# Performance work log

Hardware: AMD Instinct MI355X
Metric: run time of the kernel (lower is better)

The kernel has to match this reference:

```python
import jax, jax.numpy as jnp
import numpy as np

B, T, F, H = 64, 2048, 64, 160


def setup_inputs() -> dict:
    key = jax.random.key(0)
    ks = jax.random.split(key, 20)
    s = lambda *shape: 0.05
    inp = {
        "x": jax.random.normal(ks[0], (B, T, F), jnp.float32),
        # dilated conv weight [out=F, in=F, k=3]
        "mix_w": jax.random.normal(ks[1], (F, F, 3), jnp.float32) * 0.1,
        # batchnorm (inference) params
        "bn_g": jnp.ones((F,), jnp.float32),
        "bn_b": jnp.zeros((F,), jnp.float32),
        "bn_m": jax.random.normal(ks[2], (F,), jnp.float32) * 0.1,
        "bn_v": jax.random.uniform(ks[3], (F,), jnp.float32, 0.5, 1.5),
        # GRU1: input F -> hidden H (pytorch gate order r, z, n)
        "w_ih1": jax.random.normal(ks[4], (3 * H, F), jnp.float32) * 0.05,
        "w_hh1": jax.random.normal(ks[5], (3 * H, H), jnp.float32) * 0.05,
        "b_ih1": jax.random.normal(ks[6], (3 * H,), jnp.float32) * 0.05,
        "b_hh1": jax.random.normal(ks[7], (3 * H,), jnp.float32) * 0.05,
        # GRU2: hidden H -> hidden H
        "w_ih2": jax.random.normal(ks[8], (3 * H, H), jnp.float32) * 0.05,
        "w_hh2": jax.random.normal(ks[9], (3 * H, H), jnp.float32) * 0.05,
        "b_ih2": jax.random.normal(ks[10], (3 * H,), jnp.float32) * 0.05,
        "b_hh2": jax.random.normal(ks[11], (3 * H,), jnp.float32) * 0.05,
        # head: Linear(H, H//2) -> GELU -> (dropout=identity in eval) -> Linear(H//2, 2)
        "hw1": jax.random.normal(ks[12], (H // 2, H), jnp.float32) * 0.05,
        "hb1": jnp.zeros((H // 2,), jnp.float32),
        "hw2": jax.random.normal(ks[13], (2, H // 2), jnp.float32) * 0.05,
        "hb2": jnp.zeros((2,), jnp.float32),
    }
    return inp


def _gru(z, w_ih, w_hh, b_ih, b_hh):
    # z: [B, T, in]; returns (all hidden states [B, T, H], final hidden [B, H])
    xg = jnp.einsum('bti,gi->btg', z, w_ih) + b_ih  # [B, T, 3H]
    xg = xg.transpose(1, 0, 2)                       # [T, B, 3H]
    h0 = jnp.zeros((z.shape[0], w_hh.shape[1]), z.dtype)

    def step(h, g):
        hg = h @ w_hh.T + b_hh
        xr, xz, xn = jnp.split(g, 3, axis=-1)
        hr, hz, hn = jnp.split(hg, 3, axis=-1)
        r = jax.nn.sigmoid(xr + hr)
        u = jax.nn.sigmoid(xz + hz)
        n = jnp.tanh(xn + r * hn)
        h_new = (1.0 - u) * n + u * h
        return h_new, h_new

    hT, hs = jax.lax.scan(step, h0, xg)
    return hs.transpose(1, 0, 2), hT


def reference(x, mix_w, bn_g, bn_b, bn_m, bn_v,
              w_ih1, w_hh1, b_ih1, b_hh1,
              w_ih2, w_hh2, b_ih2, b_hh2,
              hw1, hb1, hw2, hb2):
    # dilated conv over time: x [B,T,F] -> [B,F,T]
    xc = x.transpose(0, 2, 1)
    y = jax.lax.conv_general_dilated(
        xc, mix_w, window_strides=(1,), padding=[(2, 2)],
        rhs_dilation=(2,), dimension_numbers=('NCH', 'OIH', 'NCH'))
    # batchnorm (inference) + exact GELU
    scale = bn_g / jnp.sqrt(bn_v + 1e-5)
    y = (y - bn_m[:, None]) * scale[:, None] + bn_b[:, None]
    z = jax.nn.gelu(y, approximate=False).transpose(0, 2, 1)  # [B,T,F]

    h1, _ = _gru(z, w_ih1, w_hh1, b_ih1, b_hh1)    # [B,T,H]
    _, h2T = _gru(h1, w_ih2, w_hh2, b_ih2, b_hh2)  # [B,H] (last timestep)

    q = jax.nn.gelu(h2T @ hw1.T + hb1, approximate=False)
    return q @ hw2.T + hb2  # [B, 2]
```

## Files before the change

kernel.cpp:

```cpp
#include <hip/hip_runtime.h>
#include <cmath>

#define BB 64
#define TT 2048
#define FF 64
#define HH 160
#define G3 480
#define TC 128
#define NC (TT / TC)

#define L2E  1.44269504088896340736f
#define TL2E 2.88539008177792681472f

typedef unsigned int u32;
typedef _Float16 half8 __attribute__((ext_vector_type(8)));
typedef _Float16 half2v __attribute__((ext_vector_type(2)));
typedef float f32x4 __attribute__((ext_vector_type(4)));

__device__ __forceinline__ unsigned short f2h(float v) {
    _Float16 h = (_Float16)v;
    return __builtin_bit_cast(unsigned short, h);
}
__device__ __forceinline__ u32 packh2(float a, float b) {
    return (u32)f2h(a) | ((u32)f2h(b) << 16);
}
__device__ __forceinline__ u32 packhh(_Float16 a, _Float16 b) {
    return (u32)__builtin_bit_cast(unsigned short, a)
         | ((u32)__builtin_bit_cast(unsigned short, b) << 16);
}
__device__ __forceinline__ float h2lo(u32 p) {
    return (float)__builtin_bit_cast(half2v, p)[0];
}
__device__ __forceinline__ float h2hi(u32 p) {
    return (float)__builtin_bit_cast(half2v, p)[1];
}
__device__ __forceinline__ float frcp(float v) { return __builtin_amdgcn_rcpf(v); }
#if __has_builtin(__builtin_amdgcn_exp2f)
__device__ __forceinline__ float fexp2(float v) { return __builtin_amdgcn_exp2f(v); }
#else
__device__ __forceinline__ float fexp2(float v) { return __expf(v * 0.69314718055994530942f); }
#endif
__device__ __forceinline__ float gelu_exact(float v) {
    return 0.5f * v * (1.f + erff(v * 0.70710678118654752f));
}
__device__ __forceinline__ void barrier_lgkm() {
    asm volatile("s_waitcnt lgkmcnt(0)\ns_barrier" ::: "memory");
}
__device__ __forceinline__ half8 load_wrow8(const float* p) {
    const float4* q = (const float4*)p;
    float4 a = q[0], b = q[1];
    half8 r;
    r[0] = (_Float16)a.x; r[1] = (_Float16)a.y; r[2] = (_Float16)a.z; r[3] = (_Float16)a.w;
    r[4] = (_Float16)b.x; r[5] = (_Float16)b.y; r[6] = (_Float16)b.z; r[7] = (_Float16)b.w;
    return r;
}
__device__ __forceinline__ half8 load_wrow8s(const float* p, float s) {
    const float4* q = (const float4*)p;
    float4 a = q[0], b = q[1];
    half8 r;
    r[0] = (_Float16)(a.x * s); r[1] = (_Float16)(a.y * s);
    r[2] = (_Float16)(a.z * s); r[3] = (_Float16)(a.w * s);
    r[4] = (_Float16)(b.x * s); r[5] = (_Float16)(b.y * s);
    r[6] = (_Float16)(b.z * s); r[7] = (_Float16)(b.w * s);
    return r;
}
__device__ __forceinline__ void split8(const float* v, half8& hi, half8& lo) {
    #pragma unroll
    for (int j = 0; j < 8; ++j) {
        _Float16 h = (_Float16)v[j];
        hi[j] = h;
        lo[j] = (_Float16)(v[j] - (float)h);
    }
}
#define MM16(A_, B_, C_) __builtin_amdgcn_mfma_f32_16x16x32_f16(A_, B_, C_, 0, 0, 0)

__global__ __launch_bounds__(256) void conv_mfma_kernel(
    const float* __restrict__ x, const float* __restrict__ mix_w,
    const float* __restrict__ bn_g, const float* __restrict__ bn_b,
    const float* __restrict__ bn_m, const float* __restrict__ bn_v,
    u32* __restrict__ z_out)
{
    __shared__ __align__(16) u32 xs[132 * 68];
    __shared__ __align__(8)  u32 zt[16 * 34];

    const int b   = blockIdx.y;
    const int t0  = blockIdx.x * 128;
    const int tid = threadIdx.x;
    const int wv = tid >> 6;
    const int lane = tid & 63;
    const int lane15 = lane & 15;
    const int quad = lane >> 4;

    {
        const float* xb = x + (size_t)b * TT * FF;
        for (int idx = tid; idx < 132 * 32; idx += 256) {
            const int row = idx >> 5;
            const int fp  = (idx & 31) * 2;
            const int t = t0 - 2 + row;
            float v0 = 0.f, v1 = 0.f;
            if (t >= 0 && t < TT) {
                float2 v = *(const float2*)(xb + (size_t)t * FF + fp);
                v0 = v.x; v1 = v.y;
            }
            _Float16 h0 = (_Float16)v0, h1 = (_Float16)v1;
            _Float16 l0 = (_Float16)(v0 - (float)h0);
            _Float16 l1 = (_Float16)(v1 - (float)h1);
            u32* rw = xs + row * 68;
            rw[(fp >> 1)]      = packhh(h0, h1);
            rw[32 + (fp >> 1)] = packhh(l0, l1);
        }
    }

    half8 Ahi[6], Alo[6];
    {
        const int fo = wv * 16 + lane15;
        const float* wrow = mix_w + fo * 192;
        #pragma unroll
        for (int s = 0; s < 6; ++s) {
            float wf[8];
            #pragma unroll
            for (int j = 0; j < 8; ++j) {
                int kap = s * 32 + quad * 8 + j;
                wf[j] = wrow[(kap & 63) * 3 + (kap >> 6)];
            }
            split8(wf, Ahi[s], Alo[s]);
        }
    }
    float sc[4], sh[4];
    #pragma unroll
    for (int r = 0; r < 4; ++r) {
        int f = wv * 16 + quad * 4 + r;
        float scl = bn_g[f] * rsqrtf(bn_v[f] + 1e-5f);
        sc[r] = scl; sh[r] = bn_b[f] - bn_m[f] * scl;
    }

    __syncthreads();

    u32* zrow = z_out + (size_t)(b >> 4) * TT * 512 + (b & 15) * 32;
    const int srow = tid >> 4;
    const int sc2  = tid & 15;

    for (int tt = 0; tt < 8; ++tt) {
        f32x4 C = {0.f, 0.f, 0.f, 0.f};
        #pragma unroll
        for (int s = 0; s < 6; ++s) {
            const int row = tt * 16 + lane15 + 2 * (s >> 1);
            const u32* rp = xs + row * 68 + (s & 1) * 16 + quad * 4;
            half8 Bhi = __builtin_bit_cast(half8, *(const uint4*)(rp));
            half8 Blo = __builtin_bit_cast(half8, *(const uint4*)(rp + 32));
            C = MM16(Ahi[s], Bhi, C);
            C = MM16(Ahi[s], Blo, C);
            C = MM16(Alo[s], Bhi, C);
        }
        float z0 = gelu_exact(fmaf(C[0], sc[0], sh[0]));
        float z1 = gelu_exact(fmaf(C[1], sc[1], sh[1]));
        float z2 = gelu_exact(fmaf(C[2], sc[2], sh[2]));
        float z3 = gelu_exact(fmaf(C[3], sc[3], sh[3]));
        const u32 q0 = packh2(z0, z1);
        const u32 q1 = packh2(z2, z3);
        __syncthreads();
        *(uint2*)(zt + lane15 * 34 + wv * 8 + quad * 2) = (uint2){q0, q1};
        __syncthreads();
        uint2 v = *(const uint2*)(zt + srow * 34 + sc2 * 2);
        *(uint2*)(zrow + (size_t)(t0 + tt * 16 + srow) * 512 + sc2 * 2) = v;
    }
}

#define DECLAI(i) half8 A##i##_0, A##i##_1, A##i##_2, A##i##_3, A##i##_4;
#define GLOADA(i) { int tl = wv4 + (i); int rowc = tl < 30 ? tl * 16 + lane15 : 479; \
    float sA = tl < 20 ? L2E : TL2E;                                                 \
    const float* wp = W + (size_t)rowc * K + quad * 8;                               \
    A##i##_0 = load_wrow8s(wp, sA); A##i##_1 = load_wrow8s(wp + 32, sA);             \
    if (KT > 2) { A##i##_2 = load_wrow8s(wp + 64, sA);                               \
                  A##i##_3 = load_wrow8s(wp + 96, sA);                               \
                  A##i##_4 = load_wrow8s(wp + 128, sA); }                            \
    else { A##i##_2 = A##i##_0; A##i##_3 = A##i##_0; A##i##_4 = A##i##_0; } }
#define GMM(i, kt) C##i = MM16(A##i##_##kt, Bk##kt, C##i);

template<int K, int KT, int TG>
__device__ __forceinline__ void gemm_body(
    const unsigned short* __restrict__ in,
    size_t in_blk_stride, int t_off,
    const float* __restrict__ W, const float* __restrict__ b_ih,
    const float* __restrict__ b_hh, u32* __restrict__ xg,
    int gidx, int tid)
{
    if (tid >= 512) return;
    const int wv4 = (tid >> 6) * 4;
    const int lane = tid & 63;
    const int lane15 = lane & 15;
    const int quad = lane >> 4;
    const int blk = gidx >> 4;
    const int tbase = (gidx & 15) * TG;

    DECLAI(0) DECLAI(1) DECLAI(2) DECLAI(3)
    GLOADA(0) GLOADA(1) GLOADA(2) GLOADA(3)

    f32x4 BIAS0, BIAS1, BIAS2, BIAS3;
    #define GBIAS(i) { int tl = wv4 + (i); int rowb = tl < 30 ? tl * 16 + quad * 4 : 476; \
        float sB = tl < 20 ? L2E : TL2E;                                                  \
        float4 bi = *(const float4*)(b_ih + rowb);                                        \
        if (tl < 20) { float4 bh = *(const float4*)(b_hh + rowb);                         \
            bi.x += bh.x; bi.y += bh.y; bi.z += bh.z; bi.w += bh.w; }                     \
        BIAS##i[0] = bi.x * sB; BIAS##i[1] = bi.y * sB;                                   \
        BIAS##i[2] = bi.z * sB; BIAS##i[3] = bi.w * sB; }
    GBIAS(0) GBIAS(1) GBIAS(2) GBIAS(3)
    #undef GBIAS

    const unsigned short* inb = in + (size_t)blk * in_blk_stride;
    u32* xgb = xg + (size_t)blk * TC * 3840;

    for (int t = 0; t < TG; ++t) {
        const int tt = tbase + t;
        const unsigned short* ip =
            inb + ((size_t)(t_off + tt) * 16 + lane15) * K + quad * 8;
        half8 Bk0 = __builtin_bit_cast(half8, *(const uint4*)(ip));
        half8 Bk1 = __builtin_bit_cast(half8, *(const uint4*)(ip + 32));
        half8 Bk2 = Bk0, Bk3 = Bk0, Bk4 = Bk0;
        if (KT > 2) {
            Bk2 = __builtin_bit_cast(half8, *(const uint4*)(ip + 64));
            Bk3 = __builtin_bit_cast(half8, *(const uint4*)(ip + 96));
            Bk4 = __builtin_bit_cast(half8, *(const uint4*)(ip + 128));
        }
        f32x4 C0 = BIAS0, C1 = BIAS1, C2 = BIAS2, C3 = BIAS3;
        GMM(0, 0) GMM(1, 0) GMM(2, 0) GMM(3, 0)
        GMM(0, 1) GMM(1, 1) GMM(2, 1) GMM(3, 1)
        if (KT > 2) {
            GMM(0, 2) GMM(1, 2) GMM(2, 2) GMM(3, 2)
            GMM(0, 3) GMM(1, 3) GMM(2, 3) GMM(3, 3)
            GMM(0, 4) GMM(1, 4) GMM(2, 4) GMM(3, 4)
        }
        #define GSTORE(i) { int tl = wv4 + (i); if (tl < 30) {                      \
            u32 q0 = packh2(C##i[0], C##i[1]);                                      \
            u32 q1 = packh2(C##i[2], C##i[3]);                                      \
            *(uint2*)(xgb + (((size_t)tt * 30 + tl) * 16 + lane15) * 8 + quad * 2)  \
                = (uint2){q0, q1}; } }
        GSTORE(0) GSTORE(1) GSTORE(2) GSTORE(3)
        #undef GSTORE
    }
}

#define DECLW(nm) half8 nm##0, nm##1, nm##2, nm##3, nm##4;
#define LOADWHS(nm, tb, S) { const float* wp = w_hh + (size_t)((tb) * 16 + lane15) * HH + quad * 8; \
    nm##0 = load_wrow8s(wp, S);       nm##1 = load_wrow8s(wp + 32, S);                              \
    nm##2 = load_wrow8s(wp + 64, S);  nm##3 = load_wrow8s(wp + 96, S);                              \
    nm##4 = load_wrow8s(wp + 128, S); }

template<bool WRITE_H>
__device__ __forceinline__ void scan_body(
    const u32* __restrict__ xg,
    const float* __restrict__ w_hh, const float* __restrict__ b_hh,
    float* __restrict__ h_state,
    u32* __restrict__ h_out32,
    int first, int blk, int half, int tid, uint4* h_lds)
{
    const int wv = tid >> 6;
    const int lane = tid & 63;
    const int lane15 = lane & 15;
    const int quad = lane >> 4;
    const int ch   = lane15 & 7;
    const int sel  = lane15 >> 3;
    const int ch0  = half * 8;

    DECLW(Ar) DECLW(Az) DECLW(An)
    LOADWHS(Ar, wv, L2E) LOADWHS(Az, 10 + wv, L2E) LOADWHS(An, 20 + wv, TL2E)

    const float2 bhn2 = *(const float2*)(b_hh + 320 + wv * 16 + quad * 4 + 2 * sel);
    const float bh0 = bhn2.x * TL2E, bh1 = bhn2.y * TL2E;

    float* hsp = h_state + (size_t)(blk * 16 + ch0 + ch) * HH
               + wv * 16 + quad * 4 + 2 * sel;
    float2 ho = {0.f, 0.f};
    if (!first) ho = *(const float2*)hsp;

    const int hwidx = (((2 * wv + (quad >> 1)) * 8 + ch) << 2) + 2 * (quad & 1) + sel;
    u32* hl32 = (u32*)h_lds;
    u32* HW0 = hl32 + hwidx;
    u32* HW1 = hl32 + 640 + hwidx;
    *HW0 = packh2(ho.x, ho.y);

    const int vb = 8 * quad + ch;

    const u32* xgb = xg + (size_t)blk * TC * 3840;
    const int xo_r = (((wv)      * 16 + ch0 + ch) << 3) + quad * 2 + sel;
    const int xo_z = (((10 + wv) * 16 + ch0 + ch) << 3) + quad * 2 + sel;
    const int xo_n = (((20 + wv) * 16 + ch0 + ch) << 3) + quad * 2 + sel;

    u32 xrP0 = xgb[0 * 3840 + xo_r], xzP0 = xgb[0 * 3840 + xo_z], xnP0 = xgb[0 * 3840 + xo_n];
    u32 xrP1 = xgb[1 * 3840 + xo_r], xzP1 = xgb[1 * 3840 + xo_z], xnP1 = xgb[1 * 3840 + xo_n];
    u32 xrP2 = xgb[2 * 3840 + xo_r], xzP2 = xgb[2 * 3840 + xo_z], xnP2 = xgb[2 * 3840 + xo_n];
    u32 xrP3 = xgb[3 * 3840 + xo_r], xzP3 = xgb[3 * 3840 + xo_z], xnP3 = xgb[3 * 3840 + xo_n];
    const u32* pf_r = xgb + 4 * 3840 + xo_r;
    const u32* pf_z = xgb + 4 * 3840 + xo_z;
    const u32* pf_n = xgb + 4 * 3840 + xo_n;

    u32* hp = WRITE_H
            ? h_out32 + (size_t)blk * TC * 1280 + (size_t)(ch0 + ch) * 80
              + wv * 8 + quad * 2 + sel
            : nullptr;
    __syncthreads();

    #define SCAN_STEP(RBOFF, HWP, XR, XZ, XN, PFO, HPO)                              \
    {                                                                                \
        const uint4* hb = h_lds + (RBOFF);                                           \
        uint4 b0 = hb[vb];       uint4 b1 = hb[vb + 32];                             \
        uint4 b2 = hb[vb + 64];  uint4 b3 = hb[vb + 96];                             \
        uint4 b4 = hb[vb + 128];                                                     \
        f32x4 Cr, Cz, Cn;                                                            \
        float xr0 = h2lo(XR), xr1 = h2hi(XR);                                        \
        Cr[0] = xr0; Cr[1] = xr1; Cr[2] = xr0; Cr[3] = xr1;                          \
        float xz0 = h2lo(XZ), xz1 = h2hi(XZ);                                        \
        Cz[0] = xz0; Cz[1] = xz1; Cz[2] = xz0; Cz[3] = xz1;                          \
        Cn[0] = bh0; Cn[1] = bh1; Cn[2] = bh0; Cn[3] = bh1;                          \
        float xn0 = h2lo(XN), xn1 = h2hi(XN);                                        \
        XR = pf_r[PFO]; XZ = pf_z[PFO]; XN = pf_n[PFO];                              \
        half8 B0 = __builtin_bit_cast(half8, b0);                                    \
        Cr = MM16(Ar0, B0, Cr); Cz = MM16(Az0, B0, Cz); Cn = MM16(An0, B0, Cn);      \
        half8 B1 = __builtin_bit_cast(half8, b1);                                    \
        Cr = MM16(Ar1, B1, Cr); Cz = MM16(Az1, B1, Cz); Cn = MM16(An1, B1, Cn);      \
        half8 B2 = __builtin_bit_cast(half8, b2);                                    \
        Cr = MM16(Ar2, B2, Cr); Cz = MM16(Az2, B2, Cz); Cn = MM16(An2, B2, Cn);      \
        half8 B3 = __builtin_bit_cast(half8, b3);                                    \
        Cr = MM16(Ar3, B3, Cr); Cz = MM16(Az3, B3, Cz); Cn = MM16(An3, B3, Cn);      \
        half8 B4 = __builtin_bit_cast(half8, b4);                                    \
        Cr = MM16(Ar4, B4, Cr); Cz = MM16(Az4, B4, Cz); Cn = MM16(An4, B4, Cn);      \
        {                                                                            \
            float cr0 = sel ? Cr[2] : Cr[0], cr1 = sel ? Cr[3] : Cr[1];              \
            float cz0 = sel ? Cz[2] : Cz[0], cz1 = sel ? Cz[3] : Cz[1];              \
            float cn0 = sel ? Cn[2] : Cn[0], cn1 = sel ? Cn[3] : Cn[1];              \
            float r0 = frcp(1.f + fexp2(-cr0));                                      \
            float r1 = frcp(1.f + fexp2(-cr1));                                      \
            float u0 = frcp(1.f + fexp2(-cz0));                                      \
            float u1 = frcp(1.f + fexp2(-cz1));                                      \
            float e0 = fexp2(fmaf(r0, cn0, xn0));                                    \
            float e1 = fexp2(fmaf(r1, cn1, xn1));                                    \
            float n0 = fmaf(-2.f, frcp(e0 + 1.f), 1.f);                              \
            float n1 = fmaf(-2.f, frcp(e1 + 1.f), 1.f);                              \
            ho.x = fmaf(u0, ho.x - n0, n0);                                          \
            ho.y = fmaf(u1, ho.y - n1, n1);                                          \
        }                                                                            \
        const u32 p = packh2(ho.x, ho.y);                                            \
        *(HWP) = p;                                                                  \
        if (WRITE_H) { hp[HPO] = p; }                                                \
        barrier_lgkm();                                                              \
    }

    for (int t4 = 0; t4 < TC; t4 += 4) {
        SCAN_STEP(0,   HW1, xrP0, xzP0, xnP0, 0 * 3840, 0 * 1280)
        SCAN_STEP(160, HW0, xrP1, xzP1, xnP1, 1 * 3840, 1 * 1280)
        SCAN_STEP(0,   HW1, xrP2, xzP2, xnP2, 2 * 3840, 2 * 1280)
        SCAN_STEP(160, HW0, xrP3, xzP3, xnP3, 3 * 3840, 3 * 1280)
        pf_r += 4 * 3840; pf_z += 4 * 3840; pf_n += 4 * 3840;
        if (WRITE_H) hp += 4 * 1280;
    }
    #undef SCAN_STEP

    *(float2*)hsp = ho;
}

__global__ __launch_bounds__(640, 1) void pipe_stage(
    const u32* __restrict__ z,
    u32* __restrict__ xg1,
    u32* __restrict__ xg2,
    u32* __restrict__ h1c,
    float* __restrict__ h1s, float* __restrict__ h2s,
    const float* __restrict__ w_ih1, const float* __restrict__ b_ih1,
    const float* __restrict__ w_hh1, const float* __restrict__ b_hh1,
    const float* __restrict__ w_ih2, const float* __restrict__ b_ih2,
    const float* __restrict__ w_hh2, const float* __restrict__ b_hh2,
    int k)
{
    __shared__ uint4 h_lds[2 * 160];
    const int bx = blockIdx.x;
    const int tid = threadIdx.x;
    const size_t XGCH = (size_t)4 * TC * 3840;
    const size_t H1CH = (size_t)4 * TC * 1280;

    if (bx < 8) {
        const int c = k - 1;
        if (c < 0 || c >= NC) return;
        scan_body<true>(xg1 + (c & 1) * XGCH, w_hh1, b_hh1, h1s,
                        h1c + (c & 1) * H1CH, c == 0, bx >> 1, bx & 1, tid, h_lds);
    } else if (bx < 16) {
        const int c = k - 3;
        if (c < 0 || c >= NC) return;
        scan_body<false>(xg2 + (c & 1) * XGCH, w_hh2, b_hh2, h2s,
                         nullptr, c == 0, (bx - 8) >> 1, (bx - 8) & 1, tid, h_lds);
    } else if (bx < 80) {
        const int c = k;
        if (c >= NC) return;
        gemm_body<64, 2, 8>((const unsigned short*)z, (size_t)TT * 1024, c * TC,
                            w_ih1, b_ih1, b_hh1, xg1 + (c & 1) * XGCH, bx - 16, tid);
    } else {
        const int c = k - 2;
        if (c < 0 || c >= NC) return;
        gemm_body<160, 5, 8>((const unsigned short*)(h1c + (c & 1) * H1CH),
                             (size_t)TC * 2560, 0,
                             w_ih2, b_ih2, b_hh2, xg2 + (c & 1) * XGCH, bx - 80, tid);
    }
}

__global__ __launch_bounds__(256) void head_kernel(
    const float* __restrict__ h_state,
    const float* __restrict__ hw1, const float* __restrict__ hb1,
    const float* __restrict__ hw2, const float* __restrict__ hb2,
    float* __restrict__ out)
{
    const int b = blockIdx.x;
    const int tid = threadIdx.x;
    __shared__ float hf[HH];
    __shared__ float q[80];
    if (tid < HH) hf[tid] = h_state[b * HH + tid];
    __syncthreads();
    if (tid < 80) {
        float a = hb1[tid];
        const float* wr = hw1 + (size_t)tid * HH;
        #pragma unroll 8
        for (int i = 0; i < HH; ++i) a = fmaf(wr[i], hf[i], a);
        q[tid] = gelu_exact(a);
    }
    __syncthreads();
    if (tid < 2) {
        float o = hb2[tid];
        const float* wr = hw2 + tid * 80;
        #pragma unroll 8
        for (int j = 0; j < 80; ++j) o = fmaf(wr[j], q[j], o);
        out[b * 2 + tid] = o;
    }
}

extern "C" void kernel_launch(void* const* d_in, const int* in_sizes, int n_in,
                              void* d_out, int out_size, void* d_ws, size_t ws_size,
                              hipStream_t stream)
{
    const float* x     = (const float*)d_in[0];
    const float* mix_w = (const float*)d_in[1];
    const float* bn_g  = (const float*)d_in[2];
    const float* bn_b  = (const float*)d_in[3];
    const float* bn_m  = (const float*)d_in[4];
    const float* bn_v  = (const float*)d_in[5];
    const float* w_ih1 = (const float*)d_in[6];
    const float* w_hh1 = (const float*)d_in[7];
    const float* b_ih1 = (const float*)d_in[8];
    const float* b_hh1 = (const float*)d_in[9];
    const float* w_ih2 = (const float*)d_in[10];
    const float* w_hh2 = (const float*)d_in[11];
    const float* b_ih2 = (const float*)d_in[12];
    const float* b_hh2 = (const float*)d_in[13];
    const float* hw1   = (const float*)d_in[14];
    const float* hb1   = (const float*)d_in[15];
    const float* hw2   = (const float*)d_in[16];
    const float* hb2   = (const float*)d_in[17];
    float* out = (float*)d_out;

    char* p = (char*)d_ws;
    u32* z_ws  = (u32*)p;  p += (size_t)BB * TT * 32 * 4;
    u32* xg1_ws = (u32*)p; p += (size_t)2 * 4 * TC * 3840 * 4;
    u32* xg2_ws = (u32*)p; p += (size_t)2 * 4 * TC * 3840 * 4;
    u32* h1c_ws = (u32*)p; p += (size_t)2 * 4 * TC * 1280 * 4;
    float* h1s = (float*)p; p += (size_t)BB * HH * 4;
    float* h2s = (float*)p;

    conv_mfma_kernel<<<dim3(16, BB), 256, 0, stream>>>(
        x, mix_w, bn_g, bn_b, bn_m, bn_v, z_ws);

    for (int k = 0; k <= NC + 2; ++k) {
        pipe_stage<<<144, 640, 0, stream>>>(
            z_ws, xg1_ws, xg2_ws, h1c_ws, h1s, h2s,
            w_ih1, b_ih1, w_hh1, b_hh1,
            w_ih2, b_ih2, w_hh2, b_hh2, k);
    }

    head_kernel<<<BB, 256, 0, stream>>>(h2s, hw1, hb1, hw2, hb2, out);
}
```

Measured before the change: 1.875 ms.

## Split GRU scans across 4 batch sub-blocks per group and halve conv tiles

The recurrent scan now gives each workgroup 4 batch columns instead of 8, doubling the scan blocks from 8 to 16 per GRU, so each one has a shorter per-step serial chain. Each lane computes one hidden element instead of two, with a new LDS layout for h, 16-bit stores and a changed element-select from the MFMA output. The conv kernel also uses 64-step time tiles to launch twice as many blocks. The cost is lower MFMA utilisation per block (16-wide B with only 4 distinct columns) and more blocks per pipeline launch.

New measurement: 1.615 ms. 1.16x faster.

```diff
diff --git a/kernel.cpp b/kernel.cpp
--- a/kernel.cpp
+++ b/kernel.cpp
@@ -33,6 +33,9 @@
 }
 __device__ __forceinline__ float h2hi(u32 p) {
     return (float)__builtin_bit_cast(half2v, p)[1];
+}
+__device__ __forceinline__ float h2sel(u32 p, u32 sh) {
+    return (float)__builtin_bit_cast(half2v, p >> sh)[0];
 }
 __device__ __forceinline__ float frcp(float v) { return __builtin_amdgcn_rcpf(v); }
 #if __has_builtin(__builtin_amdgcn_exp2f)
@@ -45,14 +48,6 @@
 }
 __device__ __forceinline__ void barrier_lgkm() {
     asm volatile("s_waitcnt lgkmcnt(0)\ns_barrier" ::: "memory");
-}
-__device__ __forceinline__ half8 load_wrow8(const float* p) {
-    const float4* q = (const float4*)p;
-    float4 a = q[0], b = q[1];
-    half8 r;
-    r[0] = (_Float16)a.x; r[1] = (_Float16)a.y; r[2] = (_Float16)a.z; r[3] = (_Float16)a.w;
-    r[4] = (_Float16)b.x; r[5] = (_Float16)b.y; r[6] = (_Float16)b.z; r[7] = (_Float16)b.w;
-    return r;
 }
 __device__ __forceinline__ half8 load_wrow8s(const float* p, float s) {
     const float4* q = (const float4*)p;
@@ -80,11 +75,11 @@
     const float* __restrict__ bn_m, const float* __restrict__ bn_v,
     u32* __restrict__ z_out)
 {
-    __shared__ __align__(16) u32 xs[132 * 68];
+    __shared__ __align__(16) u32 xs[68 * 68];
     __shared__ __align__(8)  u32 zt[16 * 34];
 
     const int b   = blockIdx.y;
-    const int t0  = blockIdx.x * 128;
+    const int t0  = blockIdx.x * 64;
     const int tid = threadIdx.x;
     const int wv = tid >> 6;
     const int lane = tid & 63;
@@ -93,7 +88,7 @@
 
     {
         const float* xb = x + (size_t)b * TT * FF;
-        for (int idx = tid; idx < 132 * 32; idx += 256) {
+        for (int idx = tid; idx < 68 * 32; idx += 256) {
             const int row = idx >> 5;
             const int fp  = (idx & 31) * 2;
             const int t = t0 - 2 + row;
@@ -140,7 +135,7 @@
     const int srow = tid >> 4;
     const int sc2  = tid & 15;
 
-    for (int tt = 0; tt < 8; ++tt) {
+    for (int tt = 0; tt < 4; ++tt) {
         f32x4 C = {0.f, 0.f, 0.f, 0.f};
         #pragma unroll
         for (int s = 0; s < 6; ++s) {
@@ -252,39 +247,41 @@
     const float* __restrict__ w_hh, const float* __restrict__ b_hh,
     float* __restrict__ h_state,
     u32* __restrict__ h_out32,
-    int first, int blk, int half, int tid, uint4* h_lds)
+    int first, int blk, int sub, int tid, u32* h_lds32)
 {
     const int wv = tid >> 6;
     const int lane = tid & 63;
     const int lane15 = lane & 15;
     const int quad = lane >> 4;
-    const int ch   = lane15 & 7;
-    const int sel  = lane15 >> 3;
-    const int ch0  = half * 8;
+    const int ch   = lane15 & 3;
+    const int dup  = lane15 >> 2;
+    const int ch0  = sub * 4;
+    const int row_g = wv * 16 + quad * 4 + dup;
+    const u32 shamt = (u32)(16 * (dup & 1));
+    const bool d1 = (dup & 1) != 0;
+    const bool d2 = (dup & 2) != 0;
 
     DECLW(Ar) DECLW(Az) DECLW(An)
     LOADWHS(Ar, wv, L2E) LOADWHS(Az, 10 + wv, L2E) LOADWHS(An, 20 + wv, TL2E)
 
-    const float2 bhn2 = *(const float2*)(b_hh + 320 + wv * 16 + quad * 4 + 2 * sel);
-    const float bh0 = bhn2.x * TL2E, bh1 = bhn2.y * TL2E;
-
-    float* hsp = h_state + (size_t)(blk * 16 + ch0 + ch) * HH
-               + wv * 16 + quad * 4 + 2 * sel;
-    float2 ho = {0.f, 0.f};
-    if (!first) ho = *(const float2*)hsp;
-
-    const int hwidx = (((2 * wv + (quad >> 1)) * 8 + ch) << 2) + 2 * (quad & 1) + sel;
-    u32* hl32 = (u32*)h_lds;
-    u32* HW0 = hl32 + hwidx;
-    u32* HW1 = hl32 + 640 + hwidx;
-    *HW0 = packh2(ho.x, ho.y);
-
-    const int vb = 8 * quad + ch;
+    const float bh = b_hh[320 + row_g] * TL2E;
+
+    float* hsp = h_state + (size_t)(blk * 16 + ch0 + ch) * HH + row_g;
+    float ho = first ? 0.f : *hsp;
+
+    const int widx = ch * 168 + row_g;
+    unsigned short* hw16 = (unsigned short*)h_lds32;
+    unsigned short* HW0 = hw16 + widx;
+    unsigned short* HW1 = hw16 + 672 + widx;
+    *HW0 = f2h(ho);
+
+    const int vb = ch * 21 + quad;
 
     const u32* xgb = xg + (size_t)blk * TC * 3840;
-    const int xo_r = (((wv)      * 16 + ch0 + ch) << 3) + quad * 2 + sel;
-    const int xo_z = (((10 + wv) * 16 + ch0 + ch) << 3) + quad * 2 + sel;
-    const int xo_n = (((20 + wv) * 16 + ch0 + ch) << 3) + quad * 2 + sel;
+    const int pr = quad * 2 + (dup >> 1);
+    const int xo_r = ((wv)      * 16 + ch0 + ch) * 8 + pr;
+    const int xo_z = ((10 + wv) * 16 + ch0 + ch) * 8 + pr;
+    const int xo_n = ((20 + wv) * 16 + ch0 + ch) * 8 + pr;
 
     u32 xrP0 = xgb[0 * 3840 + xo_r], xzP0 = xgb[0 * 3840 + xo_z], xnP0 = xgb[0 * 3840 + xo_n];
     u32 xrP1 = xgb[1 * 3840 + xo_r], xzP1 = xgb[1 * 3840 + xo_z], xnP1 = xgb[1 * 3840 + xo_n];
@@ -294,25 +291,24 @@
     const u32* pf_z = xgb + 4 * 3840 + xo_z;
     const u32* pf_n = xgb + 4 * 3840 + xo_n;
 
-    u32* hp = WRITE_H
-            ? h_out32 + (size_t)blk * TC * 1280 + (size_t)(ch0 + ch) * 80
-              + wv * 8 + quad * 2 + sel
+    unsigned short* hp = WRITE_H
+            ? (unsigned short*)h_out32 + (size_t)blk * TC * 2560
+              + (size_t)(ch0 + ch) * 160 + row_g
             : nullptr;
     __syncthreads();
 
     #define SCAN_STEP(RBOFF, HWP, XR, XZ, XN, PFO, HPO)                              \
     {                                                                                \
-        const uint4* hb = h_lds + (RBOFF);                                           \
-        uint4 b0 = hb[vb];       uint4 b1 = hb[vb + 32];                             \
-        uint4 b2 = hb[vb + 64];  uint4 b3 = hb[vb + 96];                             \
-        uint4 b4 = hb[vb + 128];                                                     \
-        f32x4 Cr, Cz, Cn;                                                            \
-        float xr0 = h2lo(XR), xr1 = h2hi(XR);                                        \
-        Cr[0] = xr0; Cr[1] = xr1; Cr[2] = xr0; Cr[3] = xr1;                          \
-        float xz0 = h2lo(XZ), xz1 = h2hi(XZ);                                        \
-        Cz[0] = xz0; Cz[1] = xz1; Cz[2] = xz0; Cz[3] = xz1;                          \
-        Cn[0] = bh0; Cn[1] = bh1; Cn[2] = bh0; Cn[3] = bh1;                          \
-        float xn0 = h2lo(XN), xn1 = h2hi(XN);                                        \
+        const uint4* hb = (const uint4*)(h_lds32 + (RBOFF));                         \
+        uint4 b0 = hb[vb];      uint4 b1 = hb[vb + 4];                               \
+        uint4 b2 = hb[vb + 8];  uint4 b3 = hb[vb + 12];                              \
+        uint4 b4 = hb[vb + 16];                                                      \
+        float xrv = h2sel(XR, shamt);                                                \
+        float xzv = h2sel(XZ, shamt);                                                \
+        float xnv = h2sel(XN, shamt);                                                \
+        f32x4 Cr = {xrv, xrv, xrv, xrv};                                             \
+        f32x4 Cz = {xzv, xzv, xzv, xzv};                                             \
+        f32x4 Cn = {bh, bh, bh, bh};                                                 \
         XR = pf_r[PFO]; XZ = pf_z[PFO]; XN = pf_n[PFO];                              \
         half8 B0 = __builtin_bit_cast(half8, b0);                                    \
         Cr = MM16(Ar0, B0, Cr); Cz = MM16(Az0, B0, Cz); Cn = MM16(An0, B0, Cn);      \
@@ -325,37 +321,38 @@
         half8 B4 = __builtin_bit_cast(half8, b4);                                    \
         Cr = MM16(Ar4, B4, Cr); Cz = MM16(Az4, B4, Cz); Cn = MM16(An4, B4, Cn);      \
         {                                                                            \
-            float cr0 = sel ? Cr[2] : Cr[0], cr1 = sel ? Cr[3] : Cr[1];              \
-            float cz0 = sel ? Cz[2] : Cz[0], cz1 = sel ? Cz[3] : Cz[1];              \
-            float cn0 = sel ? Cn[2] : Cn[0], cn1 = sel ? Cn[3] : Cn[1];              \
-            float r0 = frcp(1.f + fexp2(-cr0));                                      \
-            float r1 = frcp(1.f + fexp2(-cr1));                                      \
-            float u0 = frcp(1.f + fexp2(-cz0));                                      \
-            float u1 = frcp(1.f + fexp2(-cz1));                                      \
-            float e0 = fexp2(fmaf(r0, cn0, xn0));                                    \
-            float e1 = fexp2(fmaf(r1, cn1, xn1));                                    \
-            float n0 = fmaf(-2.f, frcp(e0 + 1.f), 1.f);                              \
-            float n1 = fmaf(-2.f, frcp(e1 + 1.f), 1.f);                              \
-            ho.x = fmaf(u0, ho.x - n0, n0);                                          \
-            ho.y = fmaf(u1, ho.y - n1, n1);                                          \
+            float ca = d1 ? Cr[1] : Cr[0];                                           \
+            float cb = d1 ? Cr[3] : Cr[2];                                           \
+            float crv = d2 ? cb : ca;                                                \
+            ca = d1 ? Cz[1] : Cz[0];                                                 \
+            cb = d1 ? Cz[3] : Cz[2];                                                 \
+            float czv = d2 ? cb : ca;                                                \
+            ca = d1 ? Cn[1] : Cn[0];                                                 \
+            cb = d1 ? Cn[3] : Cn[2];                                                 \
+            float cnv = d2 ? cb : ca;                                                \
+            float r = frcp(1.f + fexp2(-crv));                                       \
+            float u = frcp(1.f + fexp2(-czv));                                       \
+            float e = fexp2(fmaf(r, cnv, xnv));                                      \
+            float n = fmaf(-2.f, frcp(e + 1.f), 1.f);                                \
+            ho = fmaf(u, ho - n, n);                                                 \
         }                                                                            \
-        const u32 p = packh2(ho.x, ho.y);                                            \
-        *(HWP) = p;                                                                  \
-        if (WRITE_H) { hp[HPO] = p; }                                                \
+        const unsigned short hv = f2h(ho);                                           \
+        *(HWP) = hv;                                                                 \
+        if (WRITE_H) { hp[HPO] = hv; }                                               \
         barrier_lgkm();                                                              \
     }
 
     for (int t4 = 0; t4 < TC; t4 += 4) {
-        SCAN_STEP(0,   HW1, xrP0, xzP0, xnP0, 0 * 3840, 0 * 1280)
-        SCAN_STEP(160, HW0, xrP1, xzP1, xnP1, 1 * 3840, 1 * 1280)
-        SCAN_STEP(0,   HW1, xrP2, xzP2, xnP2, 2 * 3840, 2 * 1280)
-        SCAN_STEP(160, HW0, xrP3, xzP3, xnP3, 3 * 3840, 3 * 1280)
+        SCAN_STEP(0,   HW1, xrP0, xzP0, xnP0, 0 * 3840, 0 * 2560)
+        SCAN_STEP(336, HW0, xrP1, xzP1, xnP1, 1 * 3840, 1 * 2560)
+        SCAN_STEP(0,   HW1, xrP2, xzP2, xnP2, 2 * 3840, 2 * 2560)
+        SCAN_STEP(336, HW0, xrP3, xzP3, xnP3, 3 * 3840, 3 * 2560)
         pf_r += 4 * 3840; pf_z += 4 * 3840; pf_n += 4 * 3840;
-        if (WRITE_H) hp += 4 * 1280;
+        if (WRITE_H) hp += 4 * 2560;
     }
     #undef SCAN_STEP
 
-    *(float2*)hsp = ho;
+    *hsp = ho;
 }
 
 __global__ __launch_bounds__(640, 1) void pipe_stage(
@@ -370,33 +367,33 @@
     const float* __restrict__ w_hh2, const float* __restrict__ b_hh2,
     int k)
 {
-    __shared__ uint4 h_lds[2 * 160];
+    __shared__ __align__(16) u32 h_lds32[2 * 336];
     const int bx = blockIdx.x;
     const int tid = threadIdx.x;
     const size_t XGCH = (size_t)4 * TC * 3840;
     const size_t H1CH = (size_t)4 * TC * 1280;
 
-    if (bx < 8) {
+    if (bx < 16) {
         const int c = k - 1;
         if (c < 0 || c >= NC) return;
         scan_body<true>(xg1 + (c & 1) * XGCH, w_hh1, b_hh1, h1s,
-                        h1c + (c & 1) * H1CH, c == 0, bx >> 1, bx & 1, tid, h_lds);
-    } else if (bx < 16) {
+                        h1c + (c & 1) * H1CH, c == 0, bx >> 2, bx & 3, tid, h_lds32);
+    } else if (bx < 32) {
         const int c = k - 3;
         if (c < 0 || c >= NC) return;
         scan_body<false>(xg2 + (c & 1) * XGCH, w_hh2, b_hh2, h2s,
-                         nullptr, c == 0, (bx - 8) >> 1, (bx - 8) & 1, tid, h_lds);
-    } else if (bx < 80) {
+                         nullptr, c == 0, (bx - 16) >> 2, (bx - 16) & 3, tid, h_lds32);
+    } else if (bx < 96) {
         const int c = k;
         if (c >= NC) return;
         gemm_body<64, 2, 8>((const unsigned short*)z, (size_t)TT * 1024, c * TC,
-                            w_ih1, b_ih1, b_hh1, xg1 + (c & 1) * XGCH, bx - 16, tid);
+                            w_ih1, b_ih1, b_hh1, xg1 + (c & 1) * XGCH, bx - 32, tid);
     } else {
         const int c = k - 2;
         if (c < 0 || c >= NC) return;
         gemm_body<160, 5, 8>((const unsigned short*)(h1c + (c & 1) * H1CH),
                              (size_t)TC * 2560, 0,
-                             w_ih2, b_ih2, b_hh2, xg2 + (c & 1) * XGCH, bx - 80, tid);
+                             w_ih2, b_ih2, b_hh2, xg2 + (c & 1) * XGCH, bx - 96, tid);
     }
 }
 
@@ -461,11 +458,11 @@
     float* h1s = (float*)p; p += (size_t)BB * HH * 4;
     float* h2s = (float*)p;
 
-    conv_mfma_kernel<<<dim3(16, BB), 256, 0, stream>>>(
+    conv_mfma_kernel<<<dim3(32, BB), 256, 0, stream>>>(
         x, mix_w, bn_g, bn_b, bn_m, bn_v, z_ws);
 
     for (int k = 0; k <= NC + 2; ++k) {
-        pipe_stage<<<144, 640, 0, stream>>>(
+        pipe_stage<<<160, 640, 0, stream>>>(
             z_ws, xg1_ws, xg2_ws, h1c_ws, h1s, h2s,
             w_ih1, b_ih1, w_hh1, b_hh1,
             w_ih2, b_ih2, w_hh2, b_hh2, k);
```
